# Kernel optimization log

Measured on AMD Instinct MI355X. Metric: run time of the kernel, lower is better.

The kernel has to match this reference:

```python
import jax, jax.numpy as jnp
import numpy as np
from jax import lax

KERNEL = 3
ALPHA = 0.85
C1 = 0.01 ** 2
C2 = 0.03 ** 2


def _avg_pool(x, k):
    # stride-1 VALID average pool over the last two (H, W) dims of NCHW input
    s = lax.reduce_window(x, 0.0, lax.add, (1, 1, k, k), (1, 1, 1, 1), 'VALID')
    return s / (k * k)


def setup_inputs() -> dict:
    key = jax.random.key(0)
    k1, k2 = jax.random.split(key)
    shape = (4, 3, 1080, 1920)
    pred = jax.random.uniform(k1, shape, dtype=jnp.float32)
    gt = jax.random.uniform(k2, shape, dtype=jnp.float32)
    return {"pred": pred, "gt": gt}


def reference(pred, gt):
    p = (KERNEL - 1) // 2
    # reflection pad H and W
    x = jnp.pad(pred, ((0, 0), (0, 0), (p, p), (p, p)), mode='reflect')
    y = jnp.pad(gt, ((0, 0), (0, 0), (p, p), (p, p)), mode='reflect')

    mu_x = _avg_pool(x, KERNEL)
    mu_y = _avg_pool(y, KERNEL)
    sigma_x = _avg_pool(x * x, KERNEL) - mu_x * mu_x
    sigma_y = _avg_pool(y * y, KERNEL) - mu_y * mu_y
    sigma_xy = _avg_pool(x * y, KERNEL) - mu_x * mu_y

    ssim_n = (2.0 * mu_x * mu_y + C1) * (2.0 * sigma_xy + C2)
    ssim_d = (mu_x * mu_x + mu_y * mu_y + C1) * (sigma_x + sigma_y + C2)
    ssim_pp = jnp.clip((1.0 - ssim_n / ssim_d) * 0.5, 0.0, 1.0)

    ssim_loss = jnp.mean(ssim_pp, axis=1, keepdims=True)   # [B,1,H,W]
    l1_loss = jnp.mean(jnp.abs(pred - gt), axis=1, keepdims=True)
    return ALPHA * ssim_loss + (1.0 - ALPHA) * l1_loss
```

## Files before the change

kernel.cpp:

```cpp
#include <hip/hip_runtime.h>

#define IMG_H 1080
#define IMG_W 1920
#define CH 3

typedef float f32x2 __attribute__((ext_vector_type(2)));

#if __has_builtin(__builtin_elementwise_fma)
#define FMA2(a, b, c) __builtin_elementwise_fma((a), (b), (c))
#else
#define FMA2(a, b, c) ((a) * (b) + (c))
#endif

__device__ __forceinline__ float dpp_up1(float x) {
    int i = __float_as_int(x);
    return __int_as_float(__builtin_amdgcn_update_dpp(i, i, 0x138, 0xF, 0xF, false));
}
__device__ __forceinline__ float dpp_dn1(float x) {
    int i = __float_as_int(x);
    return __int_as_float(__builtin_amdgcn_update_dpp(i, i, 0x130, 0xF, 0xF, false));
}

__global__ __launch_bounds__(256)
void dssim_l1_kernel(const float* __restrict__ pred,
                     const float* __restrict__ gt,
                     float* __restrict__ out) {
    constexpr float K1 = 81.0f * 0.0001f;
    constexpr float K2 = 81.0f * 0.0009f;

    const f32x2 k1_ = K1, k2_ = K2;
    const f32x2 two_ = 2.0f, m2_ = -2.0f, e18_ = 18.0f, n9_ = 9.0f;
    const f32x2 mh_ = -0.5f, h_ = 0.5f, zero_ = 0.0f, one_ = 1.0f;
    const f32x2 a3_ = 0.85f / 3.0f, b3_ = 0.15f / 3.0f;

    const int lane = threadIdx.x;
    const int r0   = (blockIdx.y * 4 + threadIdx.y) * 2;
    const int b    = blockIdx.z;
    const int c0   = blockIdx.x * 128 + 2 * lane;

    const int rws[4] = { (r0 == 0) ? 1 : r0 - 1,
                         r0, r0 + 1,
                         (r0 + 2 == IMG_H) ? IMG_H - 2 : r0 + 2 };

    const bool l0 = (lane == 0), l63 = (lane == 63);
    const bool limg = l0  && (blockIdx.x == 0);
    const bool rimg = l63 && (blockIdx.x == 14);
    const int  hcol = l0 ? max(c0 - 1, 0) : min(c0 + 2, IMG_W - 1);
    const bool is_edge = l0 || l63;

    const size_t img = (size_t)IMG_H * IMG_W;
    const float* __restrict__ pb[2 * CH] = {
        pred + (size_t)b * CH * img,
        pred + (size_t)b * CH * img + img,
        pred + (size_t)b * CH * img + 2 * img,
        gt   + (size_t)b * CH * img,
        gt   + (size_t)b * CH * img + img,
        gt   + (size_t)b * CH * img + 2 * img };

    unsigned off[4];
#pragma unroll
    for (int i = 0; i < 4; ++i) off[i] = (unsigned)rws[i] * IMG_W + (unsigned)c0;

    float hx[4][CH], hy[4][CH];
    if (is_edge) {
        const unsigned hbase = (unsigned)hcol - (unsigned)c0;
#pragma unroll
        for (int i = 0; i < 4; ++i) {
            const unsigned ho = off[i] + hbase;
#pragma unroll
            for (int c = 0; c < CH; ++c) {
                hx[i][c] = pb[c][ho];
                hy[i][c] = pb[CH + c][ho];
            }
        }
    }

    f32x2 qx[4][CH], qy[4][CH];
#pragma unroll
    for (int i = 0; i < 4; ++i) {
#pragma unroll
        for (int c = 0; c < CH; ++c) {
            qx[i][c] = *reinterpret_cast<const f32x2*>(pb[c]      + off[i]);
            qy[i][c] = *reinterpret_cast<const f32x2*>(pb[CH + c] + off[i]);
        }
    }

    f32x2 Ax[CH], Ay[CH], Aw[CH], Ap[CH];
    f32x2 Bx[CH], By[CH], Bw[CH], Bp[CH];

#define CONSUME(I, DOA, FIRSTA, DOB, FIRSTB)                                \
    _Pragma("unroll")                                                       \
    for (int c = 0; c < CH; ++c) {                                          \
        const f32x2 qxv = qx[I][c], qyv = qy[I][c];                         \
        float xm = dpp_up1(qxv.y), ym = dpp_up1(qyv.y);                     \
        float xp = dpp_dn1(qxv.x), yp = dpp_dn1(qyv.x);                     \
        if (l0)   { xm = hx[I][c]; ym = hy[I][c]; }                         \
        if (l63)  { xp = hx[I][c]; yp = hy[I][c]; }                         \
        if (limg) { xm = qxv.y; ym = qyv.y; }            \
        if (rimg) { xp = qxv.x; yp = qyv.x; }       \
        const f32x2 X0 = { xm, qxv.x }, X2 = { qxv.y, xp };                 \
        const f32x2 Y0 = { ym, qyv.x }, Y2 = { qyv.y, yp };                 \
        const f32x2 WX = X0 + qxv + X2;                                     \
        const f32x2 WY = Y0 + qyv + Y2;                                     \
        const f32x2 WP = FMA2(X2, Y2, FMA2(qxv, qyv, X0 * Y0));             \
        const f32x2 WW = FMA2(X2, X2, FMA2(Y2, Y2, FMA2(qxv, qxv,           \
                         FMA2(qyv, qyv, FMA2(X0, X0, Y0 * Y0)))));          \
        if (DOA) {                                                          \
            if (FIRSTA) { Ax[c] = WX; Ay[c] = WY; Aw[c] = WW; Ap[c] = WP; } \
            else        { Ax[c] += WX; Ay[c] += WY;                         \
                          Aw[c] += WW; Ap[c] += WP; }                       \
        }                                                                   \
        if (DOB) {                                                          \
            if (FIRSTB) { Bx[c] = WX; By[c] = WY; Bw[c] = WW; Bp[c] = WP; } \
            else        { Bx[c] += WX; By[c] += WY;                         \
                          Bw[c] += WW; Bp[c] += WP; }                       \
        }                                                                   \
    }

    CONSUME(0, true, true,  false, false)
    CONSUME(1, true, false, true,  true)
    CONSUME(2, true, false, true,  false)
    CONSUME(3, false, false, true, false)
#undef CONSUME

    f32x2 l1r0 = zero_, l1r1 = zero_;
#pragma unroll
    for (int c = 0; c < CH; ++c) {
#if __has_builtin(__builtin_elementwise_abs)
        l1r0 += __builtin_elementwise_abs(qx[1][c] - qy[1][c]);
        l1r1 += __builtin_elementwise_abs(qx[2][c] - qy[2][c]);
#else
        f32x2 d0 = qx[1][c] - qy[1][c], d1 = qx[2][c] - qy[2][c];
        d0.x = fabsf(d0.x); d0.y = fabsf(d0.y);
        d1.x = fabsf(d1.x); d1.y = fabsf(d1.y);
        l1r0 += d0; l1r1 += d1;
#endif
    }

#define SSIM2(AX, AY, AW, AP, ACC)                                          \
    {                                                                       \
        const f32x2 u  = (AX) * (AY);                                       \
        const f32x2 v  = FMA2((AY), (AY), (AX) * (AX));                     \
        const f32x2 n1 = FMA2(two_, u, k1_);                                \
        const f32x2 n2 = FMA2(e18_, (AP), FMA2(m2_, u, k2_));               \
        const f32x2 d1 = v + k1_;                                           \
        const f32x2 d2 = FMA2(n9_, (AW), k2_) - v;                          \
        const f32x2 nd = n1 * n2, dd = d1 * d2;                             \
        f32x2 rc;                                                           \
        rc.x = __builtin_amdgcn_rcpf(dd.x);                                 \
        rc.y = __builtin_amdgcn_rcpf(dd.y);                                 \
        f32x2 s = FMA2(mh_, nd * rc, h_);                                   \
        s = __builtin_elementwise_min(                                      \
                __builtin_elementwise_max(s, zero_), one_);                 \
        ACC = FMA2(a3_, s, ACC);                                            \
    }

    f32x2 o0 = b3_ * l1r0;
    f32x2 o1 = b3_ * l1r1;
#pragma unroll
    for (int c = 0; c < CH; ++c) {
        SSIM2(Ax[c], Ay[c], Aw[c], Ap[c], o0)
        SSIM2(Bx[c], By[c], Bw[c], Bp[c], o1)
    }
#undef SSIM2

    float* op = out + ((size_t)b * IMG_H + r0) * IMG_W + c0;
    *reinterpret_cast<f32x2*>(op) = o0;
    *reinterpret_cast<f32x2*>(op + IMG_W) = o1;
}

extern "C" void kernel_launch(void* const* d_in, const int* in_sizes, int n_in,
                              void* d_out, int out_size, void* d_ws, size_t ws_size,
                              hipStream_t stream) {
    const float* pred = (const float*)d_in[0];
    const float* gt   = (const float*)d_in[1];
    float* out = (float*)d_out;

    dim3 block(64, 4, 1);
    dim3 grid(IMG_W / 128, IMG_H / 8, 4);
    dssim_l1_kernel<<<grid, block, 0, stream>>>(pred, gt, out);
}
```

Before: 57.41 us.

## Stage input tiles in LDS via global_load_lds and share row halos across waves

```diff
diff --git a/kernel.cpp b/kernel.cpp
--- a/kernel.cpp
+++ b/kernel.cpp
@@ -3,6 +3,11 @@
 #define IMG_H 1080
 #define IMG_W 1920
 #define CH 3
+#define TW 128
+#define TH 8
+#define INR 10
+#define NPL 6
+#define NPR 60
 
 typedef float f32x2 __attribute__((ext_vector_type(2)));
 
@@ -21,6 +26,17 @@
     return __int_as_float(__builtin_amdgcn_update_dpp(i, i, 0x130, 0xF, 0xF, false));
 }
 
+__device__ __forceinline__ void gload16(const float* g, float* l) {
+    __builtin_amdgcn_global_load_lds(
+        (const __attribute__((address_space(1))) void*)g,
+        (__attribute__((address_space(3))) void*)l,
+        16, 0, 0);
+}
+
+__device__ __forceinline__ int reflect_row(int r) {
+    return (r < 0) ? 1 : ((r >= IMG_H) ? 2 * IMG_H - 2 - r : r);
+}
+
 __global__ __launch_bounds__(256)
 void dssim_l1_kernel(const float* __restrict__ pred,
                      const float* __restrict__ gt,
@@ -33,23 +49,19 @@
     const f32x2 mh_ = -0.5f, h_ = 0.5f, zero_ = 0.0f, one_ = 1.0f;
     const f32x2 a3_ = 0.85f / 3.0f, b3_ = 0.15f / 3.0f;
 
-    const int lane = threadIdx.x;
-    const int r0   = (blockIdx.y * 4 + threadIdx.y) * 2;
+    __shared__ float tile[NPR * TW];
+    __shared__ float hL[NPR];
+    __shared__ float hR[NPR];
+
+    const int tid  = threadIdx.x;
+    const int lane = tid & 63;
+    const int wv   = tid >> 6;
     const int b    = blockIdx.z;
-    const int c0   = blockIdx.x * 128 + 2 * lane;
-
-    const int rws[4] = { (r0 == 0) ? 1 : r0 - 1,
-                         r0, r0 + 1,
-                         (r0 + 2 == IMG_H) ? IMG_H - 2 : r0 + 2 };
-
-    const bool l0 = (lane == 0), l63 = (lane == 63);
-    const bool limg = l0  && (blockIdx.x == 0);
-    const bool rimg = l63 && (blockIdx.x == 14);
-    const int  hcol = l0 ? max(c0 - 1, 0) : min(c0 + 2, IMG_W - 1);
-    const bool is_edge = l0 || l63;
+    const int c0b  = blockIdx.x * TW;
+    const int rb   = blockIdx.y * TH - 1;
 
     const size_t img = (size_t)IMG_H * IMG_W;
-    const float* __restrict__ pb[2 * CH] = {
+    const float* __restrict__ pl[NPL] = {
         pred + (size_t)b * CH * img,
         pred + (size_t)b * CH * img + img,
         pred + (size_t)b * CH * img + 2 * img,
@@ -57,47 +69,50 @@
         gt   + (size_t)b * CH * img + img,
         gt   + (size_t)b * CH * img + 2 * img };
 
-    unsigned off[4];
-#pragma unroll
-    for (int i = 0; i < 4; ++i) off[i] = (unsigned)rws[i] * IMG_W + (unsigned)c0;
-
-    float hx[4][CH], hy[4][CH];
-    if (is_edge) {
-        const unsigned hbase = (unsigned)hcol - (unsigned)c0;
-#pragma unroll
-        for (int i = 0; i < 4; ++i) {
-            const unsigned ho = off[i] + hbase;
-#pragma unroll
-            for (int c = 0; c < CH; ++c) {
-                hx[i][c] = pb[c][ho];
-                hy[i][c] = pb[CH + c][ho];
-            }
-        }
+    const int hcL = (c0b == 0) ? 1 : c0b - 1;
+    const int hcR = (c0b + TW >= IMG_W) ? IMG_W - 2 : c0b + TW;
+    if (tid < NPR) {
+        const int p = tid / INR, li = tid % INR;
+        const int r = reflect_row(rb + li);
+        hL[tid] = pl[p][(size_t)r * IMG_W + hcL];
+    } else if (tid >= 64 && tid < 64 + NPR) {
+        const int pr = tid - 64;
+        const int p = pr / INR, li = pr % INR;
+        const int r = reflect_row(rb + li);
+        hR[pr] = pl[p][(size_t)r * IMG_W + hcR];
     }
 
-    f32x2 qx[4][CH], qy[4][CH];
-#pragma unroll
-    for (int i = 0; i < 4; ++i) {
-#pragma unroll
-        for (int c = 0; c < CH; ++c) {
-            qx[i][c] = *reinterpret_cast<const f32x2*>(pb[c]      + off[i]);
-            qy[i][c] = *reinterpret_cast<const f32x2*>(pb[CH + c] + off[i]);
-        }
+    const int npair = (wv < 3) ? 8 : 6;
+    for (int k = 0; k < npair; ++k) {
+        const int P  = 8 * wv + k;
+        const int p  = P / 5;
+        const int li = 2 * (P % 5) + (lane >> 5);
+        const int r  = reflect_row(rb + li);
+        const float* g = pl[p] + (size_t)r * IMG_W + c0b + (lane & 31) * 4;
+        gload16(g, &tile[P * 256]);
     }
+    __syncthreads();
+
+    const int cp = lane;
+    const int rp = wv;
 
     f32x2 Ax[CH], Ay[CH], Aw[CH], Ap[CH];
     f32x2 Bx[CH], By[CH], Bw[CH], Bp[CH];
+    f32x2 l1r0 = zero_, l1r1 = zero_;
 
-#define CONSUME(I, DOA, FIRSTA, DOB, FIRSTB)                                \
+#define CONSUME(I, DOA, FIRSTA, DOB, FIRSTB, L1ACC)                         \
     _Pragma("unroll")                                                       \
     for (int c = 0; c < CH; ++c) {                                          \
-        const f32x2 qxv = qx[I][c], qyv = qy[I][c];                         \
+        const int li_ = 2 * rp + (I);                                       \
+        const int prx = c * INR + li_;                                      \
+        const int pry = (c + CH) * INR + li_;                               \
+        const f32x2 qxv = *reinterpret_cast<const f32x2*>(&tile[prx * TW + 2 * cp]); \
+        const f32x2 qyv = *reinterpret_cast<const f32x2*>(&tile[pry * TW + 2 * cp]); \
         float xm = dpp_up1(qxv.y), ym = dpp_up1(qyv.y);                     \
         float xp = dpp_dn1(qxv.x), yp = dpp_dn1(qyv.x);                     \
-        if (l0)   { xm = hx[I][c]; ym = hy[I][c]; }                         \
-        if (l63)  { xp = hx[I][c]; yp = hy[I][c]; }                         \
-        if (limg) { xm = qxv.y; ym = qyv.y; }            \
-        if (rimg) { xp = qxv.x; yp = qyv.x; }       \
+        if (lane == 0)  { xm = hL[prx]; ym = hL[pry]; }                     \
+        if (lane == 63) { xp = hR[prx]; yp = hR[pry]; }                     \
+        if (DOB == false && DOA == false) {}                                \
         const f32x2 X0 = { xm, qxv.x }, X2 = { qxv.y, xp };                 \
         const f32x2 Y0 = { ym, qyv.x }, Y2 = { qyv.y, yp };                 \
         const f32x2 WX = X0 + qxv + X2;                                     \
@@ -105,6 +120,11 @@
         const f32x2 WP = FMA2(X2, Y2, FMA2(qxv, qyv, X0 * Y0));             \
         const f32x2 WW = FMA2(X2, X2, FMA2(Y2, Y2, FMA2(qxv, qxv,           \
                          FMA2(qyv, qyv, FMA2(X0, X0, Y0 * Y0)))));          \
+        if (L1ACC) {                                                        \
+            f32x2 d_ = qxv - qyv;                                           \
+            d_.x = fabsf(d_.x); d_.y = fabsf(d_.y);                         \
+            *(L1ACC) += d_;                                                 \
+        }                                                                   \
         if (DOA) {                                                          \
             if (FIRSTA) { Ax[c] = WX; Ay[c] = WY; Aw[c] = WW; Ap[c] = WP; } \
             else        { Ax[c] += WX; Ay[c] += WY;                         \
@@ -117,25 +137,11 @@
         }                                                                   \
     }
 
-    CONSUME(0, true, true,  false, false)
-    CONSUME(1, true, false, true,  true)
-    CONSUME(2, true, false, true,  false)
-    CONSUME(3, false, false, true, false)
+    CONSUME(0, true, true,  false, false, ((f32x2*)0))
+    CONSUME(1, true, false, true,  true,  (&l1r0))
+    CONSUME(2, true, false, true,  false, (&l1r1))
+    CONSUME(3, false, false, true, false, ((f32x2*)0))
 #undef CONSUME
-
-    f32x2 l1r0 = zero_, l1r1 = zero_;
-#pragma unroll
-    for (int c = 0; c < CH; ++c) {
-#if __has_builtin(__builtin_elementwise_abs)
-        l1r0 += __builtin_elementwise_abs(qx[1][c] - qy[1][c]);
-        l1r1 += __builtin_elementwise_abs(qx[2][c] - qy[2][c]);
-#else
-        f32x2 d0 = qx[1][c] - qy[1][c], d1 = qx[2][c] - qy[2][c];
-        d0.x = fabsf(d0.x); d0.y = fabsf(d0.y);
-        d1.x = fabsf(d1.x); d1.y = fabsf(d1.y);
-        l1r0 += d0; l1r1 += d1;
-#endif
-    }
 
 #define SSIM2(AX, AY, AW, AP, ACC)                                          \
     {                                                                       \
@@ -164,7 +170,8 @@
     }
 #undef SSIM2
 
-    float* op = out + ((size_t)b * IMG_H + r0) * IMG_W + c0;
+    const int ro0 = blockIdx.y * TH + 2 * rp;
+    float* op = out + ((size_t)b * IMG_H + ro0) * IMG_W + c0b + 2 * cp;
     *reinterpret_cast<f32x2*>(op) = o0;
     *reinterpret_cast<f32x2*>(op + IMG_W) = o1;
 }
@@ -176,7 +183,7 @@
     const float* gt   = (const float*)d_in[1];
     float* out = (float*)d_out;
 
-    dim3 block(64, 4, 1);
-    dim3 grid(IMG_W / 128, IMG_H / 8, 4);
+    dim3 block(256, 1, 1);
+    dim3 grid(IMG_W / TW, IMG_H / TH, 4);
     dssim_l1_kernel<<<grid, block, 0, stream>>>(pred, gt, out);
 }
```

After: 71.78 us. 1.25x slower.
